# Kernel tuning notes

Measured on AMD Instinct MI355X. Metric: run time of the kernel, lower is better.

The kernel has to match this reference:

```python
import jax, jax.numpy as jnp
import numpy as np

B, S, DIN, DOUT = 4, 2048, 4096, 4096
DR, TR = 512, 64  # decomposition_rank, training_rank


def setup_inputs() -> dict:
    key = jax.random.key(0)
    ks = jax.random.split(key, 7)
    return {
        "x": jax.random.normal(ks[0], (B, S, DIN), dtype=jnp.float32),
        "u_t": jax.random.normal(ks[1], (DOUT, TR), dtype=jnp.float32) * 0.02,
        "s": jax.random.uniform(ks[2], (DR,), dtype=jnp.float32),
        "v_t": jax.random.normal(ks[3], (TR, DIN), dtype=jnp.float32) * 0.02,
        "u_d": jax.random.normal(ks[4], (DOUT, DR - TR), dtype=jnp.float32) * 0.02,
        "v_d": jax.random.normal(ks[5], (DR - TR, DIN), dtype=jnp.float32) * 0.02,
        "bias": jax.random.normal(ks[6], (DOUT,), dtype=jnp.float32) * 0.02,
    }


def reference(x, u_t, s, v_t, u_d, v_d, bias):
    tr = u_t.shape[1]  # training_rank
    # Faithful to original: materialize full [out, in] weight from scaled factors.
    siva_train = (u_t * s[:tr]) @ v_t            # [out, in]
    siva_dec = (u_d * s[tr:]) @ v_d              # [out, in]
    weight = siva_train + siva_dec               # [out, in]
    # F.linear: x @ weight.T + bias
    return jnp.einsum('bsi,oi->bso', x, weight) + bias
```

## Files before the change

kernel.cpp:

```cpp
#include <hip/hip_runtime.h>

typedef __bf16 bf16;
typedef unsigned int u32;
typedef __attribute__((ext_vector_type(4))) float f32x4;
typedef __attribute__((ext_vector_type(8))) __bf16 bf16x8;
typedef __attribute__((ext_vector_type(4))) __bf16 bf16x4;

#define MFMA_(a, b, c) __builtin_amdgcn_mfma_f32_16x16x32_bf16((a), (b), (c), 0, 0, 0)

#define DIN 4096
#define DOUT 4096
#define DR 512

__device__ __forceinline__ void gll16(const void* g, void* l) {
  __builtin_amdgcn_global_load_lds((const __attribute__((address_space(1))) u32*)g,
                                   (__attribute__((address_space(3))) u32*)l, 16, 0, 0);
}

#define FENCE() asm volatile("" ::: "memory")
#define SCHEDB() __builtin_amdgcn_sched_barrier(0)
#define WAITVM8() do { SCHEDB(); asm volatile("s_waitcnt vmcnt(8)" ::: "memory"); } while (0)
#define WAITLGKM0() asm volatile("s_waitcnt lgkmcnt(0)" ::: "memory")
#define BARRIER() do { FENCE(); __builtin_amdgcn_s_barrier(); SCHEDB(); } while (0)

__global__ __launch_bounds__(256) void prep_v_kernel(const float* __restrict__ vt,
                                                     const float* __restrict__ vd,
                                                     bf16* __restrict__ Vb) {
  int idx = blockIdx.x * 256 + threadIdx.x;
  int e = idx * 4;
  int r = e >> 12, c = e & 4095;
  const float* src = (r < 64) ? (vt + ((size_t)r << 12) + c) : (vd + ((size_t)(r - 64) << 12) + c);
  float4 v = *reinterpret_cast<const float4*>(src);
  bf16x4 o = {(bf16)v.x, (bf16)v.y, (bf16)v.z, (bf16)v.w};
  *reinterpret_cast<bf16x4*>(Vb + e) = o;
}

__global__ __launch_bounds__(256) void prep_u_kernel(const float* __restrict__ ut,
                                                     const float* __restrict__ ud,
                                                     const float* __restrict__ s,
                                                     bf16* __restrict__ Ub) {
  int idx = blockIdx.x * 256 + threadIdx.x;
  int o = idx >> 7;
  int rr = (idx & 127) * 4;
  const float* src = (rr < 64) ? (ut + (size_t)o * 64 + rr) : (ud + (size_t)o * 448 + (rr - 64));
  float4 v = *reinterpret_cast<const float4*>(src);
  float4 sv = *reinterpret_cast<const float4*>(s + rr);
  bf16x4 ov = {(bf16)(v.x * sv.x), (bf16)(v.y * sv.y), (bf16)(v.z * sv.z), (bf16)(v.w * sv.w)};
  *reinterpret_cast<bf16x4*>(Ub + (size_t)o * DR + rr) = ov;
}

__global__ __launch_bounds__(256) void gemm1_kernel(const float* __restrict__ X,
                                                    const bf16* __restrict__ Vb,
                                                    bf16* __restrict__ T) {
  __shared__ alignas(16) bf16 As[4 * 2048];
  __shared__ alignas(16) bf16 Bs[4 * 4096];

  const int tid = threadIdx.x, bid = blockIdx.x;
  const int xcd = bid & 7, slot = bid >> 3;
  const int mt = xcd * 16 + (slot >> 2), nt = slot & 3;
  const int m0 = mt * 64, n0 = nt * 128;

  const int wid = tid >> 6, lane = tid & 63;
  const int wr = wid >> 1, wc = wid & 1;
  const int lr = lane & 15, kg = lane >> 4;
  const int ks = kg ^ ((lr >> 1) & 3);

  const int arow = tid >> 2, asl = tid & 3;
  const int aphys = asl ^ ((arow >> 1) & 3);
  const float* aG = X + (size_t)(m0 + arow) * DIN + asl * 8;
  const int awoff = (arow * 4 + aphys) * 8;

  const int c0 = wid * 2, c1 = wid * 2 + 1;
  const int srcsl = (lane & 3) ^ ((lane >> 3) & 3);
  const bf16* bG0 = Vb + (size_t)(n0 + c0 * 16 + (lane >> 2)) * DIN + srcsl * 8;
  const bf16* bG1 = Vb + (size_t)(n0 + c1 * 16 + (lane >> 2)) * DIN + srcsl * 8;

  int aoff[2], boff[4];
#pragma unroll
  for (int mi = 0; mi < 2; ++mi) aoff[mi] = ((wr * 32 + mi * 16 + lr) * 4 + ks) * 8;
#pragma unroll
  for (int ni = 0; ni < 4; ++ni) boff[ni] = ((wc * 64 + ni * 16 + lr) * 4 + ks) * 8;

  f32x4 acc[2][4];
  const f32x4 z = {0.f, 0.f, 0.f, 0.f};
#pragma unroll
  for (int i = 0; i < 2; ++i)
#pragma unroll
    for (int j = 0; j < 4; ++j) acc[i][j] = z;

  float4 rA[4][2];

  rA[0][0] = *reinterpret_cast<const float4*>(aG);
  rA[0][1] = *reinterpret_cast<const float4*>(aG + 4);
  SCHEDB();
  gll16(bG0, &Bs[0 * 4096 + c0 * 512]);
  gll16(bG1, &Bs[0 * 4096 + c1 * 512]);
  rA[1][0] = *reinterpret_cast<const float4*>(aG + 32);
  rA[1][1] = *reinterpret_cast<const float4*>(aG + 36);
  SCHEDB();
  gll16(bG0 + 32, &Bs[1 * 4096 + c0 * 512]);
  gll16(bG1 + 32, &Bs[1 * 4096 + c1 * 512]);
  rA[2][0] = *reinterpret_cast<const float4*>(aG + 64);
  rA[2][1] = *reinterpret_cast<const float4*>(aG + 68);
  WAITVM8();
  {
    float4 v0 = rA[0][0], v1 = rA[0][1];
    bf16x8 w = {(bf16)v0.x, (bf16)v0.y, (bf16)v0.z, (bf16)v0.w,
                (bf16)v1.x, (bf16)v1.y, (bf16)v1.z, (bf16)v1.w};
    *reinterpret_cast<bf16x8*>(&As[0 * 2048 + awoff]) = w;
  }

#define G1_BODY(t, RB, WB, PB, SW, SP)                                               \
  do {                                                                               \
    const int kt2 = ((t) + 2 < 128) ? (t) + 2 : 127;                                 \
    const int kt3 = ((t) + 3 < 128) ? (t) + 3 : 127;                                 \
    gll16(bG0 + (size_t)kt2 * 32, &Bs[(PB) * 4096 + c0 * 512]);                      \
    gll16(bG1 + (size_t)kt2 * 32, &Bs[(PB) * 4096 + c1 * 512]);                      \
    rA[SP][0] = *reinterpret_cast<const float4*>(aG + (size_t)kt3 * 32);             \
    rA[SP][1] = *reinterpret_cast<const float4*>(aG + (size_t)kt3 * 32 + 4);         \
    WAITVM8();                                              \
    {                                                                                \
      float4 v0 = rA[SW][0], v1 = rA[SW][1];                                         \
      bf16x8 w = {(bf16)v0.x, (bf16)v0.y, (bf16)v0.z, (bf16)v0.w,                    \
                  (bf16)v1.x, (bf16)v1.y, (bf16)v1.z, (bf16)v1.w};                   \
      *reinterpret_cast<bf16x8*>(&As[(WB) * 2048 + awoff]) = w;                      \
    }                                                                                \
    WAITLGKM0();                                                                     \
    BARRIER();                                                                       \
    bf16x8 afr[2], bfr[4];                                                           \
    afr[0] = *reinterpret_cast<const bf16x8*>(&As[(RB) * 2048 + aoff[0]]);           \
    afr[1] = *reinterpret_cast<const bf16x8*>(&As[(RB) * 2048 + aoff[1]]);           \
    bfr[0] = *reinterpret_cast<const bf16x8*>(&Bs[(RB) * 4096 + boff[0]]);           \
    bfr[1] = *reinterpret_cast<const bf16x8*>(&Bs[(RB) * 4096 + boff[1]]);           \
    bfr[2] = *reinterpret_cast<const bf16x8*>(&Bs[(RB) * 4096 + boff[2]]);           \
    bfr[3] = *reinterpret_cast<const bf16x8*>(&Bs[(RB) * 4096 + boff[3]]);           \
    _Pragma("unroll") for (int mi = 0; mi < 2; ++mi)                                 \
        _Pragma("unroll") for (int ni = 0; ni < 4; ++ni)                             \
            acc[mi][ni] = MFMA_(afr[mi], bfr[ni], acc[mi][ni]);                      \
  } while (0)

  for (int tb = 0; tb < 128; tb += 4) {
    G1_BODY(tb + 0, 0, 1, 2, 1, 3);
    G1_BODY(tb + 1, 1, 2, 3, 2, 0);
    G1_BODY(tb + 2, 2, 3, 0, 3, 1);
    G1_BODY(tb + 3, 3, 0, 1, 0, 2);
  }
#undef G1_BODY

#pragma unroll
  for (int mi = 0; mi < 2; ++mi) {
    const int rbase = m0 + wr * 32 + mi * 16 + kg * 4;
#pragma unroll
    for (int ni = 0; ni < 4; ++ni) {
      const int c = n0 + wc * 64 + ni * 16 + lr;
      f32x4 a = acc[mi][ni];
#pragma unroll
      for (int j = 0; j < 4; ++j)
        T[(size_t)(rbase + j) * DR + c] = (bf16)a[j];
    }
  }
}

__global__ __launch_bounds__(256) void gemm2_kernel(const bf16* __restrict__ Tt,
                                                    const bf16* __restrict__ Ub,
                                                    const float* __restrict__ bias,
                                                    float* __restrict__ Out) {
  __shared__ alignas(16) bf16 As[4 * 4096];
  __shared__ alignas(16) bf16 Bs[4 * 4096];

  const int tid = threadIdx.x;
  const int id = ((blockIdx.x & 7) << 8) | (blockIdx.x >> 3);
  const int mt = id >> 5, nt = id & 31;
  const int m0 = mt * 128, n0 = nt * 128;

  const int wid = tid >> 6, lane = tid & 63;
  const int wr = wid >> 1, wc = wid & 1;
  const int lr = lane & 15, kg = lane >> 4;
  const int ks = kg ^ ((lr >> 1) & 3);

  const int c0 = wid * 2, c1 = wid * 2 + 1;
  const int srcsl = (lane & 3) ^ ((lane >> 3) & 3);
  const bf16* aG0 = Tt + (size_t)(m0 + c0 * 16 + (lane >> 2)) * DR + srcsl * 8;
  const bf16* aG1 = Tt + (size_t)(m0 + c1 * 16 + (lane >> 2)) * DR + srcsl * 8;
  const bf16* bG0 = Ub + (size_t)(n0 + c0 * 16 + (lane >> 2)) * DR + srcsl * 8;
  const bf16* bG1 = Ub + (size_t)(n0 + c1 * 16 + (lane >> 2)) * DR + srcsl * 8;

  int aoff[4], boff[4];
#pragma unroll
  for (int mi = 0; mi < 4; ++mi) aoff[mi] = ((wr * 64 + mi * 16 + lr) * 4 + ks) * 8;
#pragma unroll
  for (int ni = 0; ni < 4; ++ni) boff[ni] = ((wc * 64 + ni * 16 + lr) * 4 + ks) * 8;

  f32x4 acc[4][4];
  const f32x4 z = {0.f, 0.f, 0.f, 0.f};
#pragma unroll
  for (int i = 0; i < 4; ++i)
#pragma unroll
    for (int j = 0; j < 4; ++j) acc[i][j] = z;

  gll16(aG0, &As[0 * 4096 + c0 * 512]);
  gll16(aG1, &As[0 * 4096 + c1 * 512]);
  gll16(bG0, &Bs[0 * 4096 + c0 * 512]);
  gll16(bG1, &Bs[0 * 4096 + c1 * 512]);
  SCHEDB();
  gll16(aG0 + 32, &As[1 * 4096 + c0 * 512]);
  gll16(aG1 + 32, &As[1 * 4096 + c1 * 512]);
  gll16(bG0 + 32, &Bs[1 * 4096 + c0 * 512]);
  gll16(bG1 + 32, &Bs[1 * 4096 + c1 * 512]);
  SCHEDB();

#define G2_BODY(t, RB, PB)                                                           \
  do {                                                                               \
    const int kt2 = ((t) + 2 < 16) ? (t) + 2 : 15;                                   \
    gll16(aG0 + (size_t)kt2 * 32, &As[(PB) * 4096 + c0 * 512]);                      \
    gll16(aG1 + (size_t)kt2 * 32, &As[(PB) * 4096 + c1 * 512]);                      \
    gll16(bG0 + (size_t)kt2 * 32, &Bs[(PB) * 4096 + c0 * 512]);                      \
    gll16(bG1 + (size_t)kt2 * 32, &Bs[(PB) * 4096 + c1 * 512]);                      \
    WAITVM8();                                                      \
    BARRIER();                                                                       \
    bf16x8 afr[4], bfr[4];                                                           \
    _Pragma("unroll") for (int mi = 0; mi < 4; ++mi)                                 \
        afr[mi] = *reinterpret_cast<const bf16x8*>(&As[(RB) * 4096 + aoff[mi]]);     \
    _Pragma("unroll") for (int ni = 0; ni < 4; ++ni)                                 \
        bfr[ni] = *reinterpret_cast<const bf16x8*>(&Bs[(RB) * 4096 + boff[ni]]);     \
    _Pragma("unroll") for (int mi = 0; mi < 4; ++mi)                                 \
        _Pragma("unroll") for (int ni = 0; ni < 4; ++ni)                             \
            acc[mi][ni] = MFMA_(afr[mi], bfr[ni], acc[mi][ni]);                      \
  } while (0)

  for (int tb = 0; tb < 16; tb += 4) {
    G2_BODY(tb + 0, 0, 2);
    G2_BODY(tb + 1, 1, 3);
    G2_BODY(tb + 2, 2, 0);
    G2_BODY(tb + 3, 3, 1);
  }
#undef G2_BODY

#pragma unroll
  for (int ni = 0; ni < 4; ++ni) {
    const int c = n0 + wc * 64 + ni * 16 + lr;
    const float bv = bias[c];
#pragma unroll
    for (int mi = 0; mi < 4; ++mi) {
      const int rbase = m0 + wr * 64 + mi * 16 + kg * 4;
      f32x4 a = acc[mi][ni];
#pragma unroll
      for (int j = 0; j < 4; ++j)
        Out[(size_t)(rbase + j) * DOUT + c] = a[j] + bv;
    }
  }
}

extern "C" void kernel_launch(void* const* d_in, const int* in_sizes, int n_in,
                              void* d_out, int out_size, void* d_ws, size_t ws_size,
                              hipStream_t stream) {
  const float* x = (const float*)d_in[0];
  const float* u_t = (const float*)d_in[1];
  const float* s = (const float*)d_in[2];
  const float* v_t = (const float*)d_in[3];
  const float* u_d = (const float*)d_in[4];
  const float* v_d = (const float*)d_in[5];
  const float* bias = (const float*)d_in[6];
  float* out = (float*)d_out;

  bf16* Vb = (bf16*)d_ws;
  bf16* Ub = (bf16*)((char*)d_ws + (4u << 20));
  bf16* T = (bf16*)((char*)d_ws + (8u << 20));

  hipLaunchKernelGGL(prep_v_kernel, dim3(2048), dim3(256), 0, stream, v_t, v_d, Vb);
  hipLaunchKernelGGL(prep_u_kernel, dim3(2048), dim3(256), 0, stream, u_t, u_d, s, Ub);
  hipLaunchKernelGGL(gemm1_kernel, dim3(512), dim3(256), 0, stream, x, Vb, T);
  hipLaunchKernelGGL(gemm2_kernel, dim3(2048), dim3(256), 0, stream, T, Ub, bias, out);
}
```

Baseline: 387.6 us.

## Widen gemm1 tiles to full rank so X is read once per row block

```diff
diff --git a/kernel.cpp b/kernel.cpp
--- a/kernel.cpp
+++ b/kernel.cpp
@@ -19,7 +19,7 @@
 
 #define FENCE() asm volatile("" ::: "memory")
 #define SCHEDB() __builtin_amdgcn_sched_barrier(0)
-#define WAITVM8() do { SCHEDB(); asm volatile("s_waitcnt vmcnt(8)" ::: "memory"); } while (0)
+#define WAITVM(n) do { SCHEDB(); asm volatile("s_waitcnt vmcnt(" #n ")" ::: "memory"); } while (0)
 #define WAITLGKM0() asm volatile("s_waitcnt lgkmcnt(0)" ::: "memory")
 #define BARRIER() do { FENCE(); __builtin_amdgcn_s_barrier(); SCHEDB(); } while (0)
 
@@ -49,93 +49,92 @@
   *reinterpret_cast<bf16x4*>(Ub + (size_t)o * DR + rr) = ov;
 }
 
-__global__ __launch_bounds__(256) void gemm1_kernel(const float* __restrict__ X,
+__global__ __launch_bounds__(512) void gemm1_kernel(const float* __restrict__ X,
                                                     const bf16* __restrict__ Vb,
                                                     bf16* __restrict__ T) {
   __shared__ alignas(16) bf16 As[4 * 2048];
-  __shared__ alignas(16) bf16 Bs[4 * 4096];
-
-  const int tid = threadIdx.x, bid = blockIdx.x;
-  const int xcd = bid & 7, slot = bid >> 3;
-  const int mt = xcd * 16 + (slot >> 2), nt = slot & 3;
-  const int m0 = mt * 64, n0 = nt * 128;
+  __shared__ alignas(16) bf16 Bs[4 * 16384];
+
+  const int tid = threadIdx.x;
+  const int m0 = blockIdx.x * 64;
 
   const int wid = tid >> 6, lane = tid & 63;
-  const int wr = wid >> 1, wc = wid & 1;
+  const int wr = wid >> 2, wc = wid & 3;
   const int lr = lane & 15, kg = lane >> 4;
-  const int ks = kg ^ ((lr >> 1) & 3);
-
-  const int arow = tid >> 2, asl = tid & 3;
-  const int aphys = asl ^ ((arow >> 1) & 3);
-  const float* aG = X + (size_t)(m0 + arow) * DIN + asl * 8;
-  const int awoff = (arow * 4 + aphys) * 8;
-
-  const int c0 = wid * 2, c1 = wid * 2 + 1;
+  const int ksw = kg ^ ((lr >> 1) & 3);
+
+  const int arow = tid >> 3, aq = tid & 7;
+  const int as_ = aq >> 1, ah = aq & 1;
+  const int aphys = as_ ^ ((arow >> 1) & 3);
+  const float* aG = X + (size_t)(m0 + arow) * DIN + aq * 4;
+  const int awoff = arow * 32 + aphys * 8 + ah * 4;
+
   const int srcsl = (lane & 3) ^ ((lane >> 3) & 3);
-  const bf16* bG0 = Vb + (size_t)(n0 + c0 * 16 + (lane >> 2)) * DIN + srcsl * 8;
-  const bf16* bG1 = Vb + (size_t)(n0 + c1 * 16 + (lane >> 2)) * DIN + srcsl * 8;
-
-  int aoff[2], boff[4];
-#pragma unroll
-  for (int mi = 0; mi < 2; ++mi) aoff[mi] = ((wr * 32 + mi * 16 + lr) * 4 + ks) * 8;
-#pragma unroll
-  for (int ni = 0; ni < 4; ++ni) boff[ni] = ((wc * 64 + ni * 16 + lr) * 4 + ks) * 8;
-
-  f32x4 acc[2][4];
+  const int rl = lane >> 2;
+  const bf16* bG[4];
+  int bL[4];
+#pragma unroll
+  for (int i = 0; i < 4; ++i) {
+    const int c = wid * 4 + i;
+    bG[i] = Vb + (size_t)(c * 16 + rl) * DIN + srcsl * 8;
+    bL[i] = c * 512;
+  }
+
+  int aoff[2], boff[8];
+#pragma unroll
+  for (int mi = 0; mi < 2; ++mi) aoff[mi] = (wr * 32 + mi * 16 + lr) * 32 + ksw * 8;
+#pragma unroll
+  for (int ni = 0; ni < 8; ++ni) boff[ni] = (wc * 128 + ni * 16 + lr) * 32 + ksw * 8;
+
+  f32x4 acc[2][8];
   const f32x4 z = {0.f, 0.f, 0.f, 0.f};
 #pragma unroll
   for (int i = 0; i < 2; ++i)
 #pragma unroll
-    for (int j = 0; j < 4; ++j) acc[i][j] = z;
-
-  float4 rA[4][2];
-
-  rA[0][0] = *reinterpret_cast<const float4*>(aG);
-  rA[0][1] = *reinterpret_cast<const float4*>(aG + 4);
-  SCHEDB();
-  gll16(bG0, &Bs[0 * 4096 + c0 * 512]);
-  gll16(bG1, &Bs[0 * 4096 + c1 * 512]);
-  rA[1][0] = *reinterpret_cast<const float4*>(aG + 32);
-  rA[1][1] = *reinterpret_cast<const float4*>(aG + 36);
-  SCHEDB();
-  gll16(bG0 + 32, &Bs[1 * 4096 + c0 * 512]);
-  gll16(bG1 + 32, &Bs[1 * 4096 + c1 * 512]);
-  rA[2][0] = *reinterpret_cast<const float4*>(aG + 64);
-  rA[2][1] = *reinterpret_cast<const float4*>(aG + 68);
-  WAITVM8();
+    for (int j = 0; j < 8; ++j) acc[i][j] = z;
+
+  float4 rA[4];
+
+  rA[0] = *reinterpret_cast<const float4*>(aG);
+  SCHEDB();
+#pragma unroll
+  for (int i = 0; i < 4; ++i) gll16(bG[i], &Bs[0 * 16384 + bL[i]]);
+  SCHEDB();
+  rA[1] = *reinterpret_cast<const float4*>(aG + 32);
+  SCHEDB();
+#pragma unroll
+  for (int i = 0; i < 4; ++i) gll16(bG[i] + 32, &Bs[1 * 16384 + bL[i]]);
+  SCHEDB();
+  rA[2] = *reinterpret_cast<const float4*>(aG + 64);
+  WAITVM(10);
   {
-    float4 v0 = rA[0][0], v1 = rA[0][1];
-    bf16x8 w = {(bf16)v0.x, (bf16)v0.y, (bf16)v0.z, (bf16)v0.w,
-                (bf16)v1.x, (bf16)v1.y, (bf16)v1.z, (bf16)v1.w};
-    *reinterpret_cast<bf16x8*>(&As[0 * 2048 + awoff]) = w;
+    float4 v = rA[0];
+    bf16x4 w = {(bf16)v.x, (bf16)v.y, (bf16)v.z, (bf16)v.w};
+    *reinterpret_cast<bf16x4*>(&As[0 * 2048 + awoff]) = w;
   }
 
 #define G1_BODY(t, RB, WB, PB, SW, SP)                                               \
   do {                                                                               \
     const int kt2 = ((t) + 2 < 128) ? (t) + 2 : 127;                                 \
     const int kt3 = ((t) + 3 < 128) ? (t) + 3 : 127;                                 \
-    gll16(bG0 + (size_t)kt2 * 32, &Bs[(PB) * 4096 + c0 * 512]);                      \
-    gll16(bG1 + (size_t)kt2 * 32, &Bs[(PB) * 4096 + c1 * 512]);                      \
-    rA[SP][0] = *reinterpret_cast<const float4*>(aG + (size_t)kt3 * 32);             \
-    rA[SP][1] = *reinterpret_cast<const float4*>(aG + (size_t)kt3 * 32 + 4);         \
-    WAITVM8();                                              \
+    _Pragma("unroll") for (int i = 0; i < 4; ++i)                                    \
+        gll16(bG[i] + (size_t)kt2 * 32, &Bs[(PB) * 16384 + bL[i]]);                  \
+    rA[SP] = *reinterpret_cast<const float4*>(aG + (size_t)kt3 * 32);                \
+    WAITVM(10);                                           \
     {                                                                                \
-      float4 v0 = rA[SW][0], v1 = rA[SW][1];                                         \
-      bf16x8 w = {(bf16)v0.x, (bf16)v0.y, (bf16)v0.z, (bf16)v0.w,                    \
-                  (bf16)v1.x, (bf16)v1.y, (bf16)v1.z, (bf16)v1.w};                   \
-      *reinterpret_cast<bf16x8*>(&As[(WB) * 2048 + awoff]) = w;                      \
+      float4 v = rA[SW];                                                             \
+      bf16x4 w = {(bf16)v.x, (bf16)v.y, (bf16)v.z, (bf16)v.w};                       \
+      *reinterpret_cast<bf16x4*>(&As[(WB) * 2048 + awoff]) = w;                      \
     }                                                                                \
     WAITLGKM0();                                                                     \
     BARRIER();                                                                       \
-    bf16x8 afr[2], bfr[4];                                                           \
-    afr[0] = *reinterpret_cast<const bf16x8*>(&As[(RB) * 2048 + aoff[0]]);           \
-    afr[1] = *reinterpret_cast<const bf16x8*>(&As[(RB) * 2048 + aoff[1]]);           \
-    bfr[0] = *reinterpret_cast<const bf16x8*>(&Bs[(RB) * 4096 + boff[0]]);           \
-    bfr[1] = *reinterpret_cast<const bf16x8*>(&Bs[(RB) * 4096 + boff[1]]);           \
-    bfr[2] = *reinterpret_cast<const bf16x8*>(&Bs[(RB) * 4096 + boff[2]]);           \
-    bfr[3] = *reinterpret_cast<const bf16x8*>(&Bs[(RB) * 4096 + boff[3]]);           \
+    bf16x8 afr[2], bfr[8];                                                           \
     _Pragma("unroll") for (int mi = 0; mi < 2; ++mi)                                 \
-        _Pragma("unroll") for (int ni = 0; ni < 4; ++ni)                             \
+        afr[mi] = *reinterpret_cast<const bf16x8*>(&As[(RB) * 2048 + aoff[mi]]);     \
+    _Pragma("unroll") for (int ni = 0; ni < 8; ++ni)                                 \
+        bfr[ni] = *reinterpret_cast<const bf16x8*>(&Bs[(RB) * 16384 + boff[ni]]);    \
+    _Pragma("unroll") for (int mi = 0; mi < 2; ++mi)                                 \
+        _Pragma("unroll") for (int ni = 0; ni < 8; ++ni)                             \
             acc[mi][ni] = MFMA_(afr[mi], bfr[ni], acc[mi][ni]);                      \
   } while (0)
 
@@ -151,8 +150,8 @@
   for (int mi = 0; mi < 2; ++mi) {
     const int rbase = m0 + wr * 32 + mi * 16 + kg * 4;
 #pragma unroll
-    for (int ni = 0; ni < 4; ++ni) {
-      const int c = n0 + wc * 64 + ni * 16 + lr;
+    for (int ni = 0; ni < 8; ++ni) {
+      const int c = wc * 128 + ni * 16 + lr;
       f32x4 a = acc[mi][ni];
 #pragma unroll
       for (int j = 0; j < 4; ++j)
@@ -169,8 +168,10 @@
   __shared__ alignas(16) bf16 Bs[4 * 4096];
 
   const int tid = threadIdx.x;
-  const int id = ((blockIdx.x & 7) << 8) | (blockIdx.x >> 3);
-  const int mt = id >> 5, nt = id & 31;
+  const int xcd = blockIdx.x & 7;
+  const int idx = blockIdx.x >> 3;
+  const int nt = xcd * 4 + (idx & 3);
+  const int mt = idx >> 2;
   const int m0 = mt * 128, n0 = nt * 128;
 
   const int wid = tid >> 6, lane = tid & 63;
@@ -216,7 +217,7 @@
     gll16(aG1 + (size_t)kt2 * 32, &As[(PB) * 4096 + c1 * 512]);                      \
     gll16(bG0 + (size_t)kt2 * 32, &Bs[(PB) * 4096 + c0 * 512]);                      \
     gll16(bG1 + (size_t)kt2 * 32, &Bs[(PB) * 4096 + c1 * 512]);                      \
-    WAITVM8();                                                      \
+    WAITVM(8);                                                      \
     BARRIER();                                                                       \
     bf16x8 afr[4], bfr[4];                                                           \
     _Pragma("unroll") for (int mi = 0; mi < 4; ++mi)                                 \
@@ -269,6 +270,6 @@
 
   hipLaunchKernelGGL(prep_v_kernel, dim3(2048), dim3(256), 0, stream, v_t, v_d, Vb);
   hipLaunchKernelGGL(prep_u_kernel, dim3(2048), dim3(256), 0, stream, u_t, u_d, s, Ub);
-  hipLaunchKernelGGL(gemm1_kernel, dim3(512), dim3(256), 0, stream, x, Vb, T);
+  hipLaunchKernelGGL(gemm1_kernel, dim3(128), dim3(512), 0, stream, x, Vb, T);
   hipLaunchKernelGGL(gemm2_kernel, dim3(2048), dim3(256), 0, stream, T, Ub, bias, out);
 }
```

New measurement: 432.8 us. 1.12x slower.
